# Performance work log

Measured on AMD Instinct MI355X. Metric: run time of the kernel, lower is better.

## Reference

```python
import jax, jax.numpy as jnp
import numpy as np

N_NODES = 100000


def _spmm(edge_index, edge_weight, x):
    # out[i] = sum_j A[i, j] * x[j]; row=dst=edge_index[0], col=src=edge_index[1]
    dst, src = edge_index[0], edge_index[1]
    msgs = edge_weight[:, None] * x[src]  # [E, d]
    return jax.ops.segment_sum(msgs, dst, num_segments=N_NODES)


def setup_inputs() -> dict:
    key = jax.random.key(0)
    k1, k2, k3, k4 = jax.random.split(key, 4)
    N, E, D = N_NODES, 3200000, 64
    features = jax.random.normal(k1, (N, D), dtype=jnp.float32)
    edge_weight = jax.random.uniform(k2, (E,), dtype=jnp.float32)
    dst = jax.random.randint(k3, (E,), 0, N)
    src = jax.random.randint(k4, (E,), 0, N)
    edge_index = jnp.stack([dst, src]).astype(jnp.int64)
    return {"features": features, "edge_weight": edge_weight,
            "edge_index": edge_index, "degree": 2}


def reference(features, edge_weight, edge_index, degree):
    # SGC: features = adj @ features, repeated `degree` times (no learned params)
    x = features
    for _ in range(degree):
        x = _spmm(edge_index, edge_weight, x)
    return x
```

## Files before the change

### kernel.cpp

```cpp
#include <hip/hip_runtime.h>
#include <hip/hip_fp16.h>

#define N_NODES 100000
#define DFEAT 64
#define CH 4096
#define NBK 391
#define NPB 256

__global__ __launch_bounds__(512) void sort_chunks(
    const int* __restrict__ dst, const int* __restrict__ src,
    const float* __restrict__ w,
    unsigned* __restrict__ recs_g, unsigned char* __restrict__ dloc_g,
    int* __restrict__ off_g, int E)
{
    __shared__ int  hist[NBK + 1];
    __shared__ int  cursor[NBK];
    __shared__ int  sb[512];
    __shared__ unsigned      lrec[CH];
    __shared__ unsigned char ldl[CH];

    const int chunk = blockIdx.x;
    const int base  = chunk * CH;
    const int n     = min(CH, E - base);
    const int tid   = threadIdx.x;

    for (int i = tid; i < NBK + 1; i += 512) hist[i] = 0;
    __syncthreads();

    for (int k = tid; k < n; k += 512) atomicAdd(&hist[dst[base + k] >> 8], 1);
    __syncthreads();

    int v = (tid < NBK) ? hist[tid] : 0;
    sb[tid] = v;
    __syncthreads();
    for (int o = 1; o < 512; o <<= 1) {
        int t = (tid >= o) ? sb[tid - o] : 0;
        __syncthreads();
        sb[tid] += t;
        __syncthreads();
    }
    int excl = sb[tid] - v;
    if (tid <= NBK) {
        off_g[chunk * (NBK + 1) + tid] = base + excl;
        if (tid < NBK) cursor[tid] = excl;
    }
    __syncthreads();

    for (int k = tid; k < n; k += 512) {
        int d = dst[base + k];
        int pos = atomicAdd(&cursor[d >> 8], 1);
        unsigned wq = (unsigned)__float2int_rn(w[base + k] * 32768.0f);
        if (wq > 32767u) wq = 32767u;
        lrec[pos] = (unsigned)src[base + k] | (wq << 17);
        ldl[pos]  = (unsigned char)(d & 255);
    }
    __syncthreads();

    int4* rg = (int4*)(recs_g + base);
    const int4* rl = (const int4*)lrec;
    for (int k = tid; k < ((n + 3) >> 2); k += 512) rg[k] = rl[k];
    int4* dg = (int4*)(dloc_g + base);
    const int4* dl4 = (const int4*)ldl;
    for (int k = tid; k < ((n + 15) >> 4); k += 512) dg[k] = dl4[k];
}

__global__ __launch_bounds__(64) void bucket_tot(
    const int* __restrict__ off_g, int* __restrict__ gtot, int nch)
{
    const int b = blockIdx.x;
    const int lane = threadIdx.x;
    int s = 0;
    for (int c = lane; c < nch; c += 64)
        s += off_g[c * (NBK + 1) + b + 1] - off_g[c * (NBK + 1) + b];
    for (int o = 32; o > 0; o >>= 1) s += __shfl_down(s, o, 64);
    if (lane == 0) gtot[b] = s;
}

__global__ __launch_bounds__(512) void bucket_scan(
    const int* __restrict__ gtot, int* __restrict__ gbase)
{
    __shared__ int sb[512];
    const int tid = threadIdx.x;
    int v = (tid < NBK) ? gtot[tid] : 0;
    sb[tid] = v;
    __syncthreads();
    for (int o = 1; o < 512; o <<= 1) {
        int t = (tid >= o) ? sb[tid - o] : 0;
        __syncthreads();
        sb[tid] += t;
        __syncthreads();
    }
    if (tid < NBK) gbase[tid] = sb[tid] - v;
}

__global__ __launch_bounds__(512) void build_csr(
    const int* __restrict__ off_g, const unsigned* __restrict__ recs_g,
    const unsigned char* __restrict__ dloc_g, const int* __restrict__ gbase,
    unsigned* __restrict__ edges_s, int* __restrict__ row_ptr, int nch)
{
    __shared__ int hist[NPB];
    __shared__ int cursor[NPB];
    __shared__ int sb[512];

    const int b    = blockIdx.x;
    const int tid  = threadIdx.x;
    const int grp  = tid >> 4;
    const int gl   = tid & 15;
    const int gb   = gbase[b];

    if (tid < NPB) hist[tid] = 0;
    __syncthreads();

    for (int c = grp; c < nch; c += 32) {
        int beg = off_g[c * (NBK + 1) + b];
        int end = off_g[c * (NBK + 1) + b + 1];
        for (int k = beg + gl; k < end; k += 16)
            atomicAdd(&hist[dloc_g[k]], 1);
    }
    __syncthreads();

    int v = (tid < NPB) ? hist[tid] : 0;
    sb[tid] = v;
    __syncthreads();
    for (int o = 1; o < 512; o <<= 1) {
        int t = (tid >= o) ? sb[tid - o] : 0;
        __syncthreads();
        sb[tid] += t;
        __syncthreads();
    }
    if (tid < NPB) {
        int excl = sb[tid] - v;
        row_ptr[b * NPB + tid] = gb + excl;
        cursor[tid] = gb + excl;
    }
    if (b == NBK - 1 && tid == 0) row_ptr[NBK * NPB] = gb + sb[NPB - 1];
    __syncthreads();

    for (int c = grp; c < nch; c += 32) {
        int beg = off_g[c * (NBK + 1) + b];
        int end = off_g[c * (NBK + 1) + b + 1];
        for (int k = beg + gl; k < end; k += 16) {
            int pos = atomicAdd(&cursor[dloc_g[k]], 1);
            edges_s[pos] = recs_g[k];
        }
    }
}

__global__ __launch_bounds__(256) void cast_f2h(
    const float* __restrict__ in, __half* __restrict__ out, int n2)
{
    int i = blockIdx.x * blockDim.x + threadIdx.x;
    if (i < n2) {
        float2 f = ((const float2*)in)[i];
        ((__half2*)out)[i] = __floats2half2_rn(f.x, f.y);
    }
}

template <int OUT_FP16>
__global__ __launch_bounds__(256) void spmm_csr(
    const int* __restrict__ row_ptr,
    const unsigned* __restrict__ edges,
    const __half2* __restrict__ x2,
    void* __restrict__ outv)
{
    int node = __builtin_amdgcn_readfirstlane(blockIdx.x * 4 + (int)(threadIdx.x >> 6));
    if (node >= N_NODES) return;
    int lane = threadIdx.x & 63;
    int sub  = lane & 31;
    int half = lane >> 5;

    int beg = row_ptr[node];
    int end = row_ptr[node + 1];

    float ax = 0.f, ay = 0.f;
    int e0 = beg;
    for (; e0 + 8 <= end; e0 += 8) {
        int eu = __builtin_amdgcn_readfirstlane(e0);
        unsigned q0 = edges[eu],     q1 = edges[eu + 1];
        unsigned q2 = edges[eu + 2], q3 = edges[eu + 3];
        unsigned q4 = edges[eu + 4], q5 = edges[eu + 5];
        unsigned q6 = edges[eu + 6], q7 = edges[eu + 7];
        unsigned s0 = half ? q1 : q0;
        unsigned s1 = half ? q3 : q2;
        unsigned s2 = half ? q5 : q4;
        unsigned s3 = half ? q7 : q6;
        __half2 x0 = x2[((size_t)(s0 & 0x1FFFF) << 5) + sub];
        __half2 x1 = x2[((size_t)(s1 & 0x1FFFF) << 5) + sub];
        __half2 x2v = x2[((size_t)(s2 & 0x1FFFF) << 5) + sub];
        __half2 x3 = x2[((size_t)(s3 & 0x1FFFF) << 5) + sub];
        float w0 = (float)(s0 >> 17), w1 = (float)(s1 >> 17);
        float w2 = (float)(s2 >> 17), w3 = (float)(s3 >> 17);
        ax += w0 * __low2float(x0);  ay += w0 * __high2float(x0);
        ax += w1 * __low2float(x1);  ay += w1 * __high2float(x1);
        ax += w2 * __low2float(x2v); ay += w2 * __high2float(x2v);
        ax += w3 * __low2float(x3);  ay += w3 * __high2float(x3);
    }
    for (; e0 < end; e0 += 2) {
        int e = e0 + half;
        if (e < end) {
            unsigned r = edges[e];
            __half2 xv = x2[((size_t)(r & 0x1FFFF) << 5) + sub];
            float w = (float)(r >> 17);
            ax += w * __low2float(xv);
            ay += w * __high2float(xv);
        }
    }

    ax += __shfl_xor(ax, 32, 64);
    ay += __shfl_xor(ay, 32, 64);

    if (half == 0) {
        float sx = ax * (1.0f / 32768.0f);
        float sy = ay * (1.0f / 32768.0f);
        if (OUT_FP16)
            ((__half2*)outv)[(size_t)node * 32 + sub] = __floats2half2_rn(sx, sy);
        else
            ((float2*)outv)[(size_t)node * 32 + sub] = make_float2(sx, sy);
    }
}

extern "C" void kernel_launch(void* const* d_in, const int* in_sizes, int n_in,
                              void* d_out, int out_size, void* d_ws, size_t ws_size,
                              hipStream_t stream) {
    const float* features = (const float*)d_in[0];
    const float* edge_w   = (const float*)d_in[1];
    const int*   edge_idx = (const int*)d_in[2];

    const int E = in_sizes[1];
    const int* dst = edge_idx;
    const int* src = edge_idx + E;

    const int nch = (E + CH - 1) / CH;

    char* ws = (char*)d_ws;
    unsigned*      recs_g  = (unsigned*)ws;      ws += (size_t)nch * CH * sizeof(unsigned);
    unsigned char* dloc_g  = (unsigned char*)ws; ws += (size_t)nch * CH;
    unsigned*      edges_s = (unsigned*)ws;      ws += (size_t)E * sizeof(unsigned);
    __half*        tmp_h   = (__half*)ws;        ws += (size_t)N_NODES * DFEAT * sizeof(__half);
    int*           off_g   = (int*)ws;           ws += (size_t)nch * (NBK + 1) * sizeof(int);
    int*           row_ptr = (int*)ws;           ws += (size_t)(NBK * NPB + 1) * sizeof(int);
    int*           gtot    = (int*)ws;           ws += (size_t)NBK * sizeof(int);
    int*           gbase   = (int*)ws;           ws += (size_t)NBK * sizeof(int);

    __half* features_h = (__half*)recs_g;

    float* out = (float*)d_out;

    sort_chunks<<<nch, 512, 0, stream>>>(dst, src, edge_w, recs_g, dloc_g, off_g, E);
    bucket_tot<<<NBK, 64, 0, stream>>>(off_g, gtot, nch);
    bucket_scan<<<1, 512, 0, stream>>>(gtot, gbase);
    build_csr<<<NBK, 512, 0, stream>>>(off_g, recs_g, dloc_g, gbase, edges_s, row_ptr, nch);

    const int n2 = N_NODES * DFEAT / 2;
    cast_f2h<<<(n2 + 255) / 256, 256, 0, stream>>>(features, features_h, n2);

    const int ngrid = (N_NODES + 3) / 4;
    spmm_csr<1><<<ngrid, 256, 0, stream>>>(row_ptr, edges_s, (const __half2*)features_h, tmp_h);
    spmm_csr<0><<<ngrid, 256, 0, stream>>>(row_ptr, edges_s, (const __half2*)tmp_h, out);
}
```

Before: 301.4 us.

## Split fp16 features into two column planes and prefetch edge blocks in SpMM

The fp16 feature matrix is stored as two 32-column planes of 64 bytes per node, and each SpMM block now handles one plane for four nodes. Each wavefront is split into four 16-lane groups that work on different edges, with software prefetch of the next 32 edge records. The aim is a smaller gather footprint per pass, so the L2 cache holds a plane better, plus more gathers in flight. In exchange, edge records are read twice (once per plane), the grid doubles, and each gather becomes a shorter 64-byte segment.

Result: slower. 400.7 us (+33.0%).

```diff
diff --git a/kernel.cpp b/kernel.cpp
--- a/kernel.cpp
+++ b/kernel.cpp
@@ -151,8 +151,13 @@
 {
     int i = blockIdx.x * blockDim.x + threadIdx.x;
     if (i < n2) {
+        int n  = i >> 5;
+        int j  = i & 31;
+        int pl = j >> 4;
+        int jj = j & 15;
         float2 f = ((const float2*)in)[i];
-        ((__half2*)out)[i] = __floats2half2_rn(f.x, f.y);
+        ((__half2*)out)[(size_t)pl * (N_NODES * 16) + (size_t)n * 16 + jj] =
+            __floats2half2_rn(f.x, f.y);
     }
 }
 
@@ -163,59 +168,108 @@
     const __half2* __restrict__ x2,
     void* __restrict__ outv)
 {
-    int node = __builtin_amdgcn_readfirstlane(blockIdx.x * 4 + (int)(threadIdx.x >> 6));
+    const int plane = blockIdx.x & 1;
+    int node = __builtin_amdgcn_readfirstlane(
+        ((blockIdx.x >> 1) << 2) + (int)(threadIdx.x >> 6));
     if (node >= N_NODES) return;
-    int lane = threadIdx.x & 63;
-    int sub  = lane & 31;
-    int half = lane >> 5;
-
-    int beg = row_ptr[node];
-    int end = row_ptr[node + 1];
+    const int lane = threadIdx.x & 63;
+    const int g    = lane >> 4;
+    const int gl   = lane & 15;
+
+    const __half2* __restrict__ xpl = x2 + (size_t)plane * (N_NODES * 16);
+
+    const int beg = row_ptr[node];
+    const int end = row_ptr[node + 1];
 
     float ax = 0.f, ay = 0.f;
     int e0 = beg;
-    for (; e0 + 8 <= end; e0 += 8) {
-        int eu = __builtin_amdgcn_readfirstlane(e0);
-        unsigned q0 = edges[eu],     q1 = edges[eu + 1];
-        unsigned q2 = edges[eu + 2], q3 = edges[eu + 3];
-        unsigned q4 = edges[eu + 4], q5 = edges[eu + 5];
-        unsigned q6 = edges[eu + 6], q7 = edges[eu + 7];
-        unsigned s0 = half ? q1 : q0;
-        unsigned s1 = half ? q3 : q2;
-        unsigned s2 = half ? q5 : q4;
-        unsigned s3 = half ? q7 : q6;
-        __half2 x0 = x2[((size_t)(s0 & 0x1FFFF) << 5) + sub];
-        __half2 x1 = x2[((size_t)(s1 & 0x1FFFF) << 5) + sub];
-        __half2 x2v = x2[((size_t)(s2 & 0x1FFFF) << 5) + sub];
-        __half2 x3 = x2[((size_t)(s3 & 0x1FFFF) << 5) + sub];
-        float w0 = (float)(s0 >> 17), w1 = (float)(s1 >> 17);
-        float w2 = (float)(s2 >> 17), w3 = (float)(s3 >> 17);
-        ax += w0 * __low2float(x0);  ay += w0 * __high2float(x0);
-        ax += w1 * __low2float(x1);  ay += w1 * __high2float(x1);
-        ax += w2 * __low2float(x2v); ay += w2 * __high2float(x2v);
-        ax += w3 * __low2float(x3);  ay += w3 * __high2float(x3);
-    }
-    for (; e0 < end; e0 += 2) {
-        int e = e0 + half;
-        if (e < end) {
-            unsigned r = edges[e];
-            __half2 xv = x2[((size_t)(r & 0x1FFFF) << 5) + sub];
+    const int nblk = (end - beg) >> 5;
+
+    if (nblk > 0) {
+        unsigned n0 = edges[e0 +  0 + g];
+        unsigned n1 = edges[e0 +  4 + g];
+        unsigned n2r = edges[e0 +  8 + g];
+        unsigned n3 = edges[e0 + 12 + g];
+        unsigned n4 = edges[e0 + 16 + g];
+        unsigned n5 = edges[e0 + 20 + g];
+        unsigned n6 = edges[e0 + 24 + g];
+        unsigned n7 = edges[e0 + 28 + g];
+        e0 += 32;
+
+        for (int b = 0; b < nblk; ++b) {
+            __half2 v0 = xpl[(size_t)(n0  & 0x1FFFF) * 16 + gl];
+            __half2 v1 = xpl[(size_t)(n1  & 0x1FFFF) * 16 + gl];
+            __half2 v2 = xpl[(size_t)(n2r & 0x1FFFF) * 16 + gl];
+            __half2 v3 = xpl[(size_t)(n3  & 0x1FFFF) * 16 + gl];
+            __half2 v4 = xpl[(size_t)(n4  & 0x1FFFF) * 16 + gl];
+            __half2 v5 = xpl[(size_t)(n5  & 0x1FFFF) * 16 + gl];
+            __half2 v6 = xpl[(size_t)(n6  & 0x1FFFF) * 16 + gl];
+            __half2 v7 = xpl[(size_t)(n7  & 0x1FFFF) * 16 + gl];
+
+            unsigned m0 = 0, m1 = 0, m2 = 0, m3 = 0, m4 = 0, m5 = 0, m6 = 0, m7 = 0;
+            if (b + 1 < nblk) {
+                m0 = edges[e0 +  0 + g];
+                m1 = edges[e0 +  4 + g];
+                m2 = edges[e0 +  8 + g];
+                m3 = edges[e0 + 12 + g];
+                m4 = edges[e0 + 16 + g];
+                m5 = edges[e0 + 20 + g];
+                m6 = edges[e0 + 24 + g];
+                m7 = edges[e0 + 28 + g];
+                e0 += 32;
+            }
+
+            float w0 = (float)(n0  >> 17), w1 = (float)(n1 >> 17);
+            float w2 = (float)(n2r >> 17), w3 = (float)(n3 >> 17);
+            float w4 = (float)(n4  >> 17), w5 = (float)(n5 >> 17);
+            float w6 = (float)(n6  >> 17), w7 = (float)(n7 >> 17);
+            ax += w0 * __low2float(v0);  ay += w0 * __high2float(v0);
+            ax += w1 * __low2float(v1);  ay += w1 * __high2float(v1);
+            ax += w2 * __low2float(v2);  ay += w2 * __high2float(v2);
+            ax += w3 * __low2float(v3);  ay += w3 * __high2float(v3);
+            ax += w4 * __low2float(v4);  ay += w4 * __high2float(v4);
+            ax += w5 * __low2float(v5);  ay += w5 * __high2float(v5);
+            ax += w6 * __low2float(v6);  ay += w6 * __high2float(v6);
+            ax += w7 * __low2float(v7);  ay += w7 * __high2float(v7);
+
+            n0 = m0; n1 = m1; n2r = m2; n3 = m3;
+            n4 = m4; n5 = m5; n6  = m6; n7 = m7;
+        }
+    }
+
+    for (; e0 + 4 <= end; e0 += 4) {
+        unsigned r = edges[e0 + g];
+        __half2 v = xpl[(size_t)(r & 0x1FFFF) * 16 + gl];
+        float w = (float)(r >> 17);
+        ax += w * __low2float(v);
+        ay += w * __high2float(v);
+    }
+    {
+        int rem = end - e0;
+        if (g < rem) {
+            unsigned r = edges[e0 + g];
+            __half2 v = xpl[(size_t)(r & 0x1FFFF) * 16 + gl];
             float w = (float)(r >> 17);
-            ax += w * __low2float(xv);
-            ay += w * __high2float(xv);
+            ax += w * __low2float(v);
+            ay += w * __high2float(v);
         }
     }
 
+    ax += __shfl_xor(ax, 16, 64);
     ax += __shfl_xor(ax, 32, 64);
+    ay += __shfl_xor(ay, 16, 64);
     ay += __shfl_xor(ay, 32, 64);
 
-    if (half == 0) {
+    if (g == 0) {
         float sx = ax * (1.0f / 32768.0f);
         float sy = ay * (1.0f / 32768.0f);
-        if (OUT_FP16)
-            ((__half2*)outv)[(size_t)node * 32 + sub] = __floats2half2_rn(sx, sy);
-        else
-            ((float2*)outv)[(size_t)node * 32 + sub] = make_float2(sx, sy);
+        if (OUT_FP16) {
+            ((__half2*)outv)[(size_t)plane * (N_NODES * 16) + (size_t)node * 16 + gl] =
+                __floats2half2_rn(sx, sy);
+        } else {
+            ((float2*)outv)[(size_t)node * 32 + plane * 16 + gl] =
+                make_float2(sx, sy);
+        }
     }
 }
 
@@ -254,7 +308,7 @@
     const int n2 = N_NODES * DFEAT / 2;
     cast_f2h<<<(n2 + 255) / 256, 256, 0, stream>>>(features, features_h, n2);
 
-    const int ngrid = (N_NODES + 3) / 4;
+    const int ngrid = 2 * ((N_NODES + 3) / 4);
     spmm_csr<1><<<ngrid, 256, 0, stream>>>(row_ptr, edges_s, (const __half2*)features_h, tmp_h);
     spmm_csr<0><<<ngrid, 256, 0, stream>>>(row_ptr, edges_s, (const __half2*)tmp_h, out);
 }
```
